# Optimization experiments

Hardware: AMD Instinct MI355X
Metric: run time of the kernel (lower is better)

The kernel has to match this reference:

```python
import jax, jax.numpy as jnp
import numpy as np

B, S, PLM, G = 8, 2048, 768, 256
N_WM, E_WM = 50000, 800000
N_F, E_F = B * S, 131072
K = 4


def _gnn(h, src, dst, Ws, bs, n_nodes):
    # simple GCN-style message passing: aggregate neighbor features via
    # gather (h[src]) + scatter-add (segment_sum), then linear + relu.
    for W, b in zip(Ws, bs):
        m = jax.ops.segment_sum(h[src], dst, num_segments=n_nodes)  # [n, g]
        h = jax.nn.relu((h + m) @ W + b)
    return h


def setup_inputs() -> dict:
    key = jax.random.key(0)
    ks = jax.random.split(key, 16)
    std = 0.02
    inp = {
        "text_embeddings": jax.random.normal(ks[0], (B, S, PLM), jnp.float32),
        "wm_x": jax.random.normal(ks[1], (N_WM, G), jnp.float32),
        "wm_edge_index": jax.random.randint(ks[2], (2, E_WM), 0, N_WM),
        "token2nodepos": jax.random.randint(ks[3], (B * S, K), 0, N_WM),
        "fstm_node_ids": jax.random.randint(ks[4], (N_F,), 0, N_F),
        "fstm_edge_index": jax.random.randint(ks[5], (2, E_F), 0, N_F),
        # extra_emb: nn.Embedding(2, G, padding_idx=0) -> row 0 is zeros
        "extra_emb": jax.random.normal(ks[6], (2, G), jnp.float32).at[0].set(0.0) * std,
        "wm_W1": jax.random.normal(ks[7], (G, G), jnp.float32) * std,
        "wm_b1": jnp.zeros((G,), jnp.float32),
        "wm_W2": jax.random.normal(ks[8], (G, G), jnp.float32) * std,
        "wm_b2": jnp.zeros((G,), jnp.float32),
        "fstm_W1": jax.random.normal(ks[9], (G, G), jnp.float32) * std,
        "fstm_b1": jnp.zeros((G,), jnp.float32),
        "fstm_W2": jax.random.normal(ks[10], (G, G), jnp.float32) * std,
        "fstm_b2": jnp.zeros((G,), jnp.float32),
        "fc1_W": jax.random.normal(ks[11], (G + PLM, G), jnp.float32) * std,
        "fc1_b": jnp.zeros((G,), jnp.float32),
        "fc3_W": jax.random.normal(ks[12], (PLM + 2 * G, PLM), jnp.float32) * std,
        "fc3_b": jnp.zeros((PLM,), jnp.float32),
    }
    return inp


def reference(text_embeddings, wm_x, wm_edge_index, token2nodepos, fstm_node_ids,
              fstm_edge_index, extra_emb, wm_W1, wm_b1, wm_W2, wm_b2,
              fstm_W1, fstm_b1, fstm_W2, fstm_b2, fc1_W, fc1_b, fc3_W, fc3_b):
    # ====== WM ======
    graph_embeddings = _gnn(wm_x, wm_edge_index[0], wm_edge_index[1],
                            (wm_W1, wm_W2), (wm_b1, wm_b2), N_WM)  # [N_WM, G]
    table = jnp.concatenate([extra_emb, graph_embeddings], axis=0)  # [N_WM+2, G]
    # per-token gather-sum over K concept slots (original python loop, vectorized)
    tmp = jnp.sum(table[token2nodepos + 2], axis=1)  # [B*S, G]
    text_flat = text_embeddings.reshape(B * S, PLM)
    graph_text_embed = jnp.concatenate([tmp, text_flat], axis=-1) @ fc1_W + fc1_b  # [B*S, G]
    # ====== FSTM ======
    x = graph_text_embed[fstm_node_ids]  # [B*S, G]
    temporal = _gnn(x, fstm_edge_index[0], fstm_edge_index[1],
                    (fstm_W1, fstm_W2), (fstm_b1, fstm_b2), N_F)
    temporal = temporal.reshape(B, S, G)
    # ====== Final ======
    final_vec = jnp.concatenate(
        [text_embeddings, tmp.reshape(B, S, G), temporal], axis=-1)
    logits = final_vec @ fc3_W + fc3_b  # [B, S, PLM]
    return logits
```

## Files before the change

### kernel.cpp

```cpp
#include <hip/hip_runtime.h>

#define Bsz 8
#define Ssz 2048
#define PLM 768
#define Gd  256
#define N_WM 50000
#define E_WM 800000
#define N_F  16384
#define E_F  131072
#define Kc   4

typedef unsigned short ushort_t;
typedef short short8 __attribute__((ext_vector_type(8)));
typedef float f32x4 __attribute__((ext_vector_type(4)));

__device__ __forceinline__ ushort_t f2bf(float f) {
    union { float f; unsigned int u; } v; v.f = f;
    unsigned int r = (v.u + 0x7fffu + ((v.u >> 16) & 1u)) >> 16;
    return (ushort_t)r;
}
__device__ __forceinline__ float bf2f(ushort_t b) {
    union { unsigned int u; float f; } v; v.u = ((unsigned int)b) << 16;
    return v.f;
}
__device__ __forceinline__ float4 bf4f(ushort4 u) {
    return make_float4(bf2f(u.x), bf2f(u.y), bf2f(u.z), bf2f(u.w));
}

__device__ __forceinline__ void gl2lds16(const ushort_t* g, ushort_t* l) {
    __builtin_amdgcn_global_load_lds(
        (const __attribute__((address_space(1))) unsigned int*)g,
        (__attribute__((address_space(3))) unsigned int*)l, 16, 0, 0);
}

__device__ __forceinline__ void cvt4(const float* __restrict__ in,
                                     ushort_t* __restrict__ out, int i, int n4) {
    if (i < n4) {
        float4 v = ((const float4*)in)[i];
        ushort4 u;
        u.x = f2bf(v.x); u.y = f2bf(v.y); u.z = f2bf(v.z); u.w = f2bf(v.w);
        ((ushort4*)out)[i] = u;
    }
}
__device__ __forceinline__ void wtx(const float* __restrict__ W,
                                    ushort_t* __restrict__ Wt, int K, int N, int idx) {
    if (idx < N * K) {
        int n = idx / K, k = idx % K;
        Wt[idx] = f2bf(W[(size_t)k * N + n]);
    }
}

__global__ void conv_all(const float* __restrict__ wm_x, const float* __restrict__ text,
                         const float* __restrict__ extra,
                         const float* __restrict__ W1, const float* __restrict__ W2,
                         const float* __restrict__ W3, const float* __restrict__ W4,
                         const float* __restrict__ W5, const float* __restrict__ W6,
                         ushort_t* __restrict__ Xb, ushort_t* __restrict__ Tx,
                         ushort_t* __restrict__ Exb,
                         ushort_t* __restrict__ T1, ushort_t* __restrict__ T2,
                         ushort_t* __restrict__ T3, ushort_t* __restrict__ T4,
                         ushort_t* __restrict__ T5, ushort_t* __restrict__ T6) {
    int b = blockIdx.x, t = threadIdx.x;
    if (b < 12500) { cvt4(wm_x, Xb, b * 256 + t, 3200000); return; }
    b -= 12500;
    if (b < 12288) { cvt4(text, Tx, b * 256 + t, 3145728); return; }
    b -= 12288;
    if (b < 1) { cvt4(extra, Exb, t, 128); return; }
    b -= 1;
    if (b < 256) { wtx(W1, T1, 256, 256, b * 256 + t); return; }
    b -= 256;
    if (b < 256) { wtx(W2, T2, 256, 256, b * 256 + t); return; }
    b -= 256;
    if (b < 256) { wtx(W3, T3, 256, 256, b * 256 + t); return; }
    b -= 256;
    if (b < 256) { wtx(W4, T4, 256, 256, b * 256 + t); return; }
    b -= 256;
    if (b < 1024) { wtx(W5, T5, 1024, 256, b * 256 + t); return; }
    b -= 1024;
    wtx(W6, T6, 1280, 768, b * 256 + t);
}

__global__ void hist_both(const int* __restrict__ wm_dst, int* __restrict__ wm_cnt,
                          const int* __restrict__ f_dst, int* __restrict__ fs_cnt) {
    int e = blockIdx.x * 256 + threadIdx.x;
    if (e < E_WM) {
        atomicAdd(&wm_cnt[wm_dst[e]], 1);
    } else {
        int e2 = e - E_WM;
        if (e2 < E_F) atomicAdd(&fs_cnt[f_dst[e2]], 1);
    }
}

__global__ void fill_both(const int* __restrict__ wm_src, const int* __restrict__ wm_dst,
                          int* __restrict__ wm_cur, int* __restrict__ wm_bkt,
                          const int* __restrict__ f_src, const int* __restrict__ f_dst,
                          int* __restrict__ fs_cur, int* __restrict__ fs_bkt) {
    int e = blockIdx.x * 256 + threadIdx.x;
    if (e < E_WM) {
        int p = atomicAdd(&wm_cur[wm_dst[e]], 1);
        wm_bkt[p] = wm_src[e];
    } else {
        int e2 = e - E_WM;
        if (e2 < E_F) {
            int p = atomicAdd(&fs_cur[f_dst[e2]], 1);
            fs_bkt[p] = f_src[e2];
        }
    }
}

__device__ __forceinline__ void scan1_body(const int* __restrict__ cnt,
                                           int* __restrict__ bsum, int n, int lb,
                                           int* sm) {
    int t = threadIdx.x;
    int base = lb * 1024 + t * 4;
    int s = 0;
    if (base + 3 < n) {
        int4 q = *(const int4*)&cnt[base];
        s = q.x + q.y + q.z + q.w;
    } else {
#pragma unroll
        for (int i = 0; i < 4; ++i) if (base + i < n) s += cnt[base + i];
    }
    sm[t] = s; __syncthreads();
#pragma unroll
    for (int st = 128; st > 0; st >>= 1) {
        if (t < st) sm[t] += sm[t + st];
        __syncthreads();
    }
    if (t == 0) bsum[lb] = sm[0];
}

#define NBW 49
#define NBF 16
__global__ __launch_bounds__(256) void scan1_both(const int* __restrict__ wm_cnt,
                                                  int* __restrict__ bsum_wm,
                                                  const int* __restrict__ fs_cnt,
                                                  int* __restrict__ bsum_fs) {
    __shared__ int sm[256];
    int b = blockIdx.x;
    if (b < NBW) scan1_body(wm_cnt, bsum_wm, N_WM, b, sm);
    else         scan1_body(fs_cnt, bsum_fs, N_F, b - NBW, sm);
}

__global__ void scan_bsums_both(int* __restrict__ bw, int* __restrict__ bf) {
    int w = threadIdx.x >> 6, lane = threadIdx.x & 63;
    int* b = w ? bf : bw;
    int nb = w ? NBF : NBW;
    int o = (lane < nb) ? b[lane] : 0;
    int v = o;
#pragma unroll
    for (int off = 1; off < 64; off <<= 1) {
        int t = __shfl_up(v, off, 64);
        if (lane >= off) v += t;
    }
    if (lane < nb) b[lane] = v - o;
}

__device__ __forceinline__ void scan2_body(int* __restrict__ cnt, int* __restrict__ off,
                                           const int* __restrict__ bsum, int n,
                                           int total, int lb, int* sm) {
    int t = threadIdx.x;
    int base = lb * 1024 + t * 4;
    int v0 = 0, v1 = 0, v2 = 0, v3 = 0;
    if (base + 3 < n) {
        int4 q = *(const int4*)&cnt[base];
        v0 = q.x; v1 = q.y; v2 = q.z; v3 = q.w;
    } else {
        if (base + 0 < n) v0 = cnt[base + 0];
        if (base + 1 < n) v1 = cnt[base + 1];
        if (base + 2 < n) v2 = cnt[base + 2];
        if (base + 3 < n) v3 = cnt[base + 3];
    }
    int s = v0 + v1 + v2 + v3;
    sm[t] = s;
    __syncthreads();
#pragma unroll
    for (int st = 1; st < 256; st <<= 1) {
        int x = (t >= st) ? sm[t - st] : 0;
        __syncthreads();
        sm[t] += x;
        __syncthreads();
    }
    int ex = bsum[lb] + sm[t] - s;
    int o0 = ex, o1 = ex + v0, o2 = o1 + v1, o3 = o2 + v2;
    if (base + 0 < n) { off[base + 0] = o0; cnt[base + 0] = o0; }
    if (base + 1 < n) { off[base + 1] = o1; cnt[base + 1] = o1; }
    if (base + 2 < n) { off[base + 2] = o2; cnt[base + 2] = o2; }
    if (base + 3 < n) { off[base + 3] = o3; cnt[base + 3] = o3; }
    if (lb == 0 && t == 0) off[n] = total;
}

__global__ __launch_bounds__(256) void scan2_both(int* __restrict__ wm_cnt,
                                                  int* __restrict__ wm_off,
                                                  const int* __restrict__ bsum_wm,
                                                  int* __restrict__ fs_cnt,
                                                  int* __restrict__ fs_off,
                                                  const int* __restrict__ bsum_fs) {
    __shared__ int sm[256];
    int b = blockIdx.x;
    if (b < NBW) scan2_body(wm_cnt, wm_off, bsum_wm, N_WM, E_WM, b, sm);
    else         scan2_body(fs_cnt, fs_off, bsum_fs, N_F, E_F, b - NBW, sm);
}

__global__ void aggregate_kernel(const ushort_t* __restrict__ h,
                                 const int* __restrict__ off,
                                 const int* __restrict__ bucket,
                                 ushort_t* __restrict__ hm, int n) {
    int i = blockIdx.x * 4 + (threadIdx.x >> 6);
    if (i >= n) return;
    int lane = threadIdx.x & 63;
    int s0 = off[i], s1 = off[i + 1];
    const ushort4* hp = (const ushort4*)h;
    float4 acc = bf4f(hp[(size_t)i * 64 + lane]);
    int j = s0;
    for (; j + 8 <= s1; j += 8) {
        int b0 = bucket[j + 0], b1 = bucket[j + 1];
        int b2 = bucket[j + 2], b3 = bucket[j + 3];
        int b4 = bucket[j + 4], b5 = bucket[j + 5];
        int b6 = bucket[j + 6], b7 = bucket[j + 7];
        ushort4 r0 = hp[(size_t)b0 * 64 + lane];
        ushort4 r1 = hp[(size_t)b1 * 64 + lane];
        ushort4 r2 = hp[(size_t)b2 * 64 + lane];
        ushort4 r3 = hp[(size_t)b3 * 64 + lane];
        ushort4 r4 = hp[(size_t)b4 * 64 + lane];
        ushort4 r5 = hp[(size_t)b5 * 64 + lane];
        ushort4 r6 = hp[(size_t)b6 * 64 + lane];
        ushort4 r7 = hp[(size_t)b7 * 64 + lane];
        float4 v0 = bf4f(r0), v1 = bf4f(r1), v2 = bf4f(r2), v3 = bf4f(r3);
        float4 v4 = bf4f(r4), v5 = bf4f(r5), v6 = bf4f(r6), v7 = bf4f(r7);
        acc.x += v0.x + v1.x + v2.x + v3.x + v4.x + v5.x + v6.x + v7.x;
        acc.y += v0.y + v1.y + v2.y + v3.y + v4.y + v5.y + v6.y + v7.y;
        acc.z += v0.z + v1.z + v2.z + v3.z + v4.z + v5.z + v6.z + v7.z;
        acc.w += v0.w + v1.w + v2.w + v3.w + v4.w + v5.w + v6.w + v7.w;
    }
    for (; j + 2 <= s1; j += 2) {
        int b0 = bucket[j + 0], b1 = bucket[j + 1];
        ushort4 r0 = hp[(size_t)b0 * 64 + lane];
        ushort4 r1 = hp[(size_t)b1 * 64 + lane];
        float4 v0 = bf4f(r0), v1 = bf4f(r1);
        acc.x += v0.x + v1.x; acc.y += v0.y + v1.y;
        acc.z += v0.z + v1.z; acc.w += v0.w + v1.w;
    }
    if (j < s1) {
        int b0 = bucket[j];
        float4 v0 = bf4f(hp[(size_t)b0 * 64 + lane]);
        acc.x += v0.x; acc.y += v0.y; acc.z += v0.z; acc.w += v0.w;
    }
    ushort4 u;
    u.x = f2bf(acc.x); u.y = f2bf(acc.y); u.z = f2bf(acc.z); u.w = f2bf(acc.w);
    ((ushort4*)hm)[(size_t)i * 64 + lane] = u;
}

__global__ void tmp_kernel(const ushort_t* __restrict__ gemb,
                           const ushort_t* __restrict__ extra,
                           const int* __restrict__ t2np,
                           ushort_t* __restrict__ D) {
    int i = blockIdx.x * 4 + (threadIdx.x >> 6);
    int lane = threadIdx.x & 63;
    float4 s = make_float4(0.f, 0.f, 0.f, 0.f);
#pragma unroll
    for (int k = 0; k < Kc; ++k) {
        int idx = t2np[i * Kc + k] + 2;
        const ushort4* row = (idx < 2) ? (const ushort4*)(extra + (size_t)idx * Gd)
                                       : (const ushort4*)(gemb + (size_t)(idx - 2) * Gd);
        float4 v = bf4f(row[lane]);
        s.x += v.x; s.y += v.y; s.z += v.z; s.w += v.w;
    }
    ushort4 u;
    u.x = f2bf(s.x); u.y = f2bf(s.y); u.z = f2bf(s.z); u.w = f2bf(s.w);
    ((ushort4*)D)[(size_t)i * 64 + lane] = u;
}

__global__ void gather_kernel(const ushort_t* __restrict__ Ein,
                              const int* __restrict__ ids,
                              ushort_t* __restrict__ F) {
    int i = blockIdx.x * 4 + (threadIdx.x >> 6);
    int lane = threadIdx.x & 63;
    ((ushort4*)F)[(size_t)i * 64 + lane] =
        ((const ushort4*)Ein)[(size_t)ids[i] * 64 + lane];
}

#define TBM 128
#define TBN 128
#define TBK 64

__device__ __forceinline__ void xcd_swizzle(int& bx, int& by) {
    int gx = gridDim.x;
    int nwg = gx * gridDim.y;
    int orig = by * gx + bx;
    int q = nwg >> 3, r = nwg & 7;
    int xcd = orig & 7, loc = orig >> 3;
    int wg = (xcd < r ? xcd * (q + 1) : r * (q + 1) + (xcd - r) * q) + loc;
    bx = wg % gx;
    by = wg / gx;
}

template <int MODE, int OUTBF>
__global__ __launch_bounds__(256) void mfma_gemm(
    const ushort_t* __restrict__ p0, const ushort_t* __restrict__ p1,
    const ushort_t* __restrict__ p2, const ushort_t* __restrict__ Wt,
    const float* __restrict__ bias, void* __restrict__ Cv,
    int M, int N, int K, int relu) {
    __shared__ ushort_t As[TBM * TBK];
    __shared__ ushort_t Bs[TBN * TBK];

    int tid  = threadIdx.x;
    int lane = tid & 63;
    int wave = tid >> 6;
    int wm = (wave >> 1) * 64, wn = (wave & 1) * 64;
    int bx = blockIdx.x, by = blockIdx.y;
    xcd_swizzle(bx, by);
    int row0 = by * TBM, col0 = bx * TBN;
    int l15 = lane & 15, l4 = lane >> 4;

    f32x4 acc[4][4];
#pragma unroll
    for (int i = 0; i < 4; ++i)
#pragma unroll
        for (int j = 0; j < 4; ++j)
            acc[i][j] = (f32x4){0.f, 0.f, 0.f, 0.f};

    for (int k0 = 0; k0 < K; k0 += TBK) {
#pragma unroll
        for (int it = 0; it < 4; ++it) {
            int eb = it * 2048 + wave * 512;
            int le = eb + lane * 8;
            int r  = le >> 6;
            int kl = le & 63;
            int grow = row0 + r; if (grow > M - 1) grow = M - 1;
            int gk = k0 + kl;
            const ushort_t* gp;
            if (MODE == 0)
                gp = p0 + (size_t)grow * K + gk;
            else if (MODE == 2)
                gp = (gk < 256) ? p0 + (size_t)grow * 256 + gk
                                : p1 + (size_t)grow * 768 + (gk - 256);
            else
                gp = (gk < 768) ? p0 + (size_t)grow * 768 + gk
                   : (gk < 1024) ? p1 + (size_t)grow * 256 + (gk - 768)
                                 : p2 + (size_t)grow * 256 + (gk - 1024);
            gl2lds16(gp, &As[eb]);
        }
#pragma unroll
        for (int it = 0; it < 4; ++it) {
            int eb = it * 2048 + wave * 512;
            int le = eb + lane * 8;
            int nl = le >> 6;
            int kl = le & 63;
            const ushort_t* gp = Wt + (size_t)(col0 + nl) * K + k0 + kl;
            gl2lds16(gp, &Bs[eb]);
        }
        __syncthreads();

#pragma unroll
        for (int ks = 0; ks < TBK; ks += 32) {
            short8 af[4], bfr[4];
#pragma unroll
            for (int mi = 0; mi < 4; ++mi)
                af[mi] = *(const short8*)&As[(wm + mi * 16 + l15) * TBK + ks + l4 * 8];
#pragma unroll
            for (int ni = 0; ni < 4; ++ni)
                bfr[ni] = *(const short8*)&Bs[(wn + ni * 16 + l15) * TBK + ks + l4 * 8];
#pragma unroll
            for (int mi = 0; mi < 4; ++mi)
#pragma unroll
                for (int ni = 0; ni < 4; ++ni)
                    acc[mi][ni] = __builtin_amdgcn_mfma_f32_16x16x32_bf16(
                        af[mi], bfr[ni], acc[mi][ni], 0, 0, 0);
        }
        __syncthreads();
    }

#pragma unroll
    for (int ni = 0; ni < 4; ++ni) {
        int c = col0 + wn + ni * 16 + l15;
        float bv = bias[c];
#pragma unroll
        for (int mi = 0; mi < 4; ++mi) {
#pragma unroll
            for (int r = 0; r < 4; ++r) {
                int rr = row0 + wm + mi * 16 + l4 * 4 + r;
                if (rr < M) {
                    float v = acc[mi][ni][r] + bv;
                    if (relu) v = fmaxf(v, 0.f);
                    if (OUTBF) ((ushort_t*)Cv)[(size_t)rr * N + c] = f2bf(v);
                    else       ((float*)Cv)[(size_t)rr * N + c] = v;
                }
            }
        }
    }
}

extern "C" void kernel_launch(void* const* d_in, const int* in_sizes, int n_in,
                              void* d_out, int out_size, void* d_ws, size_t ws_size,
                              hipStream_t stream) {
    const float* text    = (const float*)d_in[0];
    const float* wm_x    = (const float*)d_in[1];
    const int*   wm_ei   = (const int*)d_in[2];
    const int*   t2np    = (const int*)d_in[3];
    const int*   f_ids   = (const int*)d_in[4];
    const int*   f_ei    = (const int*)d_in[5];
    const float* extra   = (const float*)d_in[6];
    const float* wm_W1   = (const float*)d_in[7];
    const float* wm_b1   = (const float*)d_in[8];
    const float* wm_W2   = (const float*)d_in[9];
    const float* wm_b2   = (const float*)d_in[10];
    const float* fs_W1   = (const float*)d_in[11];
    const float* fs_b1   = (const float*)d_in[12];
    const float* fs_W2   = (const float*)d_in[13];
    const float* fs_b2   = (const float*)d_in[14];
    const float* fc1_W   = (const float*)d_in[15];
    const float* fc1_b   = (const float*)d_in[16];
    const float* fc3_W   = (const float*)d_in[17];
    const float* fc3_b   = (const float*)d_in[18];
    float* out = (float*)d_out;

    ushort_t* Xb  = (ushort_t*)d_ws;
    ushort_t* Ag  = Xb + 12800000;
    ushort_t* Gm  = Ag + 12800000;
    ushort_t* Tx  = Gm + 12800000;
    ushort_t* Dt  = Tx + 12582912;
    ushort_t* Ee  = Dt + 4194304;
    ushort_t* Wv  = Ee + 4194304;
    ushort_t* wt_wm1 = Wv;
    ushort_t* wt_wm2 = wt_wm1 + 65536;
    ushort_t* wt_fs1 = wt_wm2 + 65536;
    ushort_t* wt_fs2 = wt_fs1 + 65536;
    ushort_t* wt_fc1 = wt_fs2 + 65536;
    ushort_t* wt_fc3 = wt_fc1 + 262144;
    ushort_t* Exb    = wt_fc3 + 983040;
    int* wm_off = (int*)(Exb + 512);
    int* fs_off = wm_off + N_WM + 1;
    int* wm_cnt = fs_off + N_F + 1;
    int* fs_cnt = wm_cnt + N_WM;
    int* wm_bkt = fs_cnt + N_F;
    int* fs_bkt = wm_bkt + E_WM;
    int* bsum_wm = fs_bkt + E_F;
    int* bsum_fs = bsum_wm + 64;

    ushort_t* h1 = Xb;
    ushort_t* F  = Gm;
    ushort_t* H  = Gm + 4194304;
    ushort_t* T  = Ee;

    const int* wm_src = wm_ei;
    const int* wm_dst = wm_ei + E_WM;
    const int* f_src  = f_ei;
    const int* f_dst  = f_ei + E_F;

    dim3 blk(256);
    dim3 gW(Gd / TBN, (N_WM + TBM - 1) / TBM);
    dim3 gF(Gd / TBN, N_F / TBM);
    dim3 gO(PLM / TBN, N_F / TBM);

    const int nbE = (E_WM + E_F) / 256;

    hipMemsetAsync(wm_cnt, 0, (N_WM + N_F) * sizeof(int), stream);
    hist_both<<<nbE, blk, 0, stream>>>(wm_dst, wm_cnt, f_dst, fs_cnt);
    scan1_both<<<NBW + NBF, blk, 0, stream>>>(wm_cnt, bsum_wm, fs_cnt, bsum_fs);
    scan_bsums_both<<<1, 128, 0, stream>>>(bsum_wm, bsum_fs);
    scan2_both<<<NBW + NBF, blk, 0, stream>>>(wm_cnt, wm_off, bsum_wm,
                                              fs_cnt, fs_off, bsum_fs);
    fill_both<<<nbE, blk, 0, stream>>>(wm_src, wm_dst, wm_cnt, wm_bkt,
                                       f_src, f_dst, fs_cnt, fs_bkt);

    conv_all<<<30677, blk, 0, stream>>>(wm_x, text, extra,
                                        wm_W1, wm_W2, fs_W1, fs_W2, fc1_W, fc3_W,
                                        Xb, Tx, Exb,
                                        wt_wm1, wt_wm2, wt_fs1, wt_fs2,
                                        wt_fc1, wt_fc3);

    aggregate_kernel<<<(N_WM + 3) / 4, blk, 0, stream>>>(Xb, wm_off, wm_bkt, Ag, N_WM);
    mfma_gemm<0, 1><<<gW, blk, 0, stream>>>(Ag, nullptr, nullptr, wt_wm1, wm_b1,
                                            h1, N_WM, Gd, Gd, 1);
    aggregate_kernel<<<(N_WM + 3) / 4, blk, 0, stream>>>(h1, wm_off, wm_bkt, Ag, N_WM);
    mfma_gemm<0, 1><<<gW, blk, 0, stream>>>(Ag, nullptr, nullptr, wt_wm2, wm_b2,
                                            Gm, N_WM, Gd, Gd, 1);
    tmp_kernel<<<N_F / 4, blk, 0, stream>>>(Gm, Exb, t2np, Dt);
    mfma_gemm<2, 1><<<gF, blk, 0, stream>>>(Dt, Tx, nullptr, wt_fc1, fc1_b,
                                            Ee, N_F, Gd, Gd + PLM, 0);
    gather_kernel<<<N_F / 4, blk, 0, stream>>>(Ee, f_ids, F);
    aggregate_kernel<<<N_F / 4, blk, 0, stream>>>(F, fs_off, fs_bkt, Ag, N_F);
    mfma_gemm<0, 1><<<gF, blk, 0, stream>>>(Ag, nullptr, nullptr, wt_fs1, fs_b1,
                                            H, N_F, Gd, Gd, 1);
    aggregate_kernel<<<N_F / 4, blk, 0, stream>>>(H, fs_off, fs_bkt, Ag, N_F);
    mfma_gemm<0, 1><<<gF, blk, 0, stream>>>(Ag, nullptr, nullptr, wt_fs2, fs_b2,
                                            T, N_F, Gd, Gd, 1);
    mfma_gemm<3, 0><<<gO, blk, 0, stream>>>(Tx, Dt, T, wt_fc3, fc3_b,
                                            out, N_F, PLM, PLM + 2 * Gd, 0);
}
```

Before: 634.3 us.

## Build CSR via two-level bucketed counting sort with shared-memory atomics

Replaces the global-atomic histogram, three-pass scan and global-atomic fill with a two-level radix-style counting sort. Edges are first bucketed by high bits of the destination into coarse buckets using shared-memory histograms per chunk, then each coarse bucket is sorted locally in shared memory to produce offsets and bucket arrays. The aim is to cut contended global atomics and random scattered writes during CSR construction. The cost is an extra pass through an int2 staging buffer that reuses the Ag workspace, plus more kernel launches.

```diff
diff --git a/kernel.cpp b/kernel.cpp
--- a/kernel.cpp
+++ b/kernel.cpp
@@ -80,100 +80,48 @@
     wtx(W6, T6, 1280, 768, b * 256 + t);
 }
 
-__global__ void hist_both(const int* __restrict__ wm_dst, int* __restrict__ wm_cnt,
-                          const int* __restrict__ f_dst, int* __restrict__ fs_cnt) {
-    int e = blockIdx.x * 256 + threadIdx.x;
-    if (e < E_WM) {
-        atomicAdd(&wm_cnt[wm_dst[e]], 1);
+#define WM_P 512
+#define WM_CH 1563
+#define WM_SHIFT 8
+#define FS_P 128
+#define FS_CH 1024
+#define FS_SHIFT 6
+
+__global__ __launch_bounds__(256) void csr_p1(const int* __restrict__ wm_dst,
+                                              const int* __restrict__ f_dst,
+                                              int* __restrict__ Cwm,
+                                              int* __restrict__ Cfs) {
+    __shared__ int hist[256];
+    int b = blockIdx.x, t = threadIdx.x;
+    hist[t] = 0; __syncthreads();
+    if (b < WM_P) {
+        int e0 = b * WM_CH, e1 = e0 + WM_CH; if (e1 > E_WM) e1 = E_WM;
+        for (int e = e0 + t; e < e1; e += 256)
+            atomicAdd(&hist[wm_dst[e] >> WM_SHIFT], 1);
+        __syncthreads();
+        Cwm[b * 256 + t] = hist[t];
     } else {
-        int e2 = e - E_WM;
-        if (e2 < E_F) atomicAdd(&fs_cnt[f_dst[e2]], 1);
-    }
-}
-
-__global__ void fill_both(const int* __restrict__ wm_src, const int* __restrict__ wm_dst,
-                          int* __restrict__ wm_cur, int* __restrict__ wm_bkt,
-                          const int* __restrict__ f_src, const int* __restrict__ f_dst,
-                          int* __restrict__ fs_cur, int* __restrict__ fs_bkt) {
-    int e = blockIdx.x * 256 + threadIdx.x;
-    if (e < E_WM) {
-        int p = atomicAdd(&wm_cur[wm_dst[e]], 1);
-        wm_bkt[p] = wm_src[e];
-    } else {
-        int e2 = e - E_WM;
-        if (e2 < E_F) {
-            int p = atomicAdd(&fs_cur[f_dst[e2]], 1);
-            fs_bkt[p] = f_src[e2];
-        }
-    }
-}
-
-__device__ __forceinline__ void scan1_body(const int* __restrict__ cnt,
-                                           int* __restrict__ bsum, int n, int lb,
-                                           int* sm) {
-    int t = threadIdx.x;
-    int base = lb * 1024 + t * 4;
-    int s = 0;
-    if (base + 3 < n) {
-        int4 q = *(const int4*)&cnt[base];
-        s = q.x + q.y + q.z + q.w;
-    } else {
-#pragma unroll
-        for (int i = 0; i < 4; ++i) if (base + i < n) s += cnt[base + i];
-    }
+        int p = b - WM_P;
+        int e0 = p * FS_CH, e1 = e0 + FS_CH;
+        for (int e = e0 + t; e < e1; e += 256)
+            atomicAdd(&hist[f_dst[e] >> FS_SHIFT], 1);
+        __syncthreads();
+        Cfs[p * 256 + t] = hist[t];
+    }
+}
+
+__global__ __launch_bounds__(256) void csr_p2a(int* __restrict__ Cwm, int* __restrict__ BTwm,
+                                               int* __restrict__ Cfs, int* __restrict__ BTfs) {
+    __shared__ int sm[256];
+    int b = blockIdx.x, t = threadIdx.x;
+    int* C; int* BT; int P; int bk;
+    if (b < 256) { C = Cwm; BT = BTwm; P = WM_P; bk = b; }
+    else         { C = Cfs; BT = BTfs; P = FS_P; bk = b - 256; }
+    int half = P >> 1;
+    int v0 = 0, v1 = 0;
+    if (t < half) { v0 = C[(2 * t) * 256 + bk]; v1 = C[(2 * t + 1) * 256 + bk]; }
+    int s = v0 + v1;
     sm[t] = s; __syncthreads();
-#pragma unroll
-    for (int st = 128; st > 0; st >>= 1) {
-        if (t < st) sm[t] += sm[t + st];
-        __syncthreads();
-    }
-    if (t == 0) bsum[lb] = sm[0];
-}
-
-#define NBW 49
-#define NBF 16
-__global__ __launch_bounds__(256) void scan1_both(const int* __restrict__ wm_cnt,
-                                                  int* __restrict__ bsum_wm,
-                                                  const int* __restrict__ fs_cnt,
-                                                  int* __restrict__ bsum_fs) {
-    __shared__ int sm[256];
-    int b = blockIdx.x;
-    if (b < NBW) scan1_body(wm_cnt, bsum_wm, N_WM, b, sm);
-    else         scan1_body(fs_cnt, bsum_fs, N_F, b - NBW, sm);
-}
-
-__global__ void scan_bsums_both(int* __restrict__ bw, int* __restrict__ bf) {
-    int w = threadIdx.x >> 6, lane = threadIdx.x & 63;
-    int* b = w ? bf : bw;
-    int nb = w ? NBF : NBW;
-    int o = (lane < nb) ? b[lane] : 0;
-    int v = o;
-#pragma unroll
-    for (int off = 1; off < 64; off <<= 1) {
-        int t = __shfl_up(v, off, 64);
-        if (lane >= off) v += t;
-    }
-    if (lane < nb) b[lane] = v - o;
-}
-
-__device__ __forceinline__ void scan2_body(int* __restrict__ cnt, int* __restrict__ off,
-                                           const int* __restrict__ bsum, int n,
-                                           int total, int lb, int* sm) {
-    int t = threadIdx.x;
-    int base = lb * 1024 + t * 4;
-    int v0 = 0, v1 = 0, v2 = 0, v3 = 0;
-    if (base + 3 < n) {
-        int4 q = *(const int4*)&cnt[base];
-        v0 = q.x; v1 = q.y; v2 = q.z; v3 = q.w;
-    } else {
-        if (base + 0 < n) v0 = cnt[base + 0];
-        if (base + 1 < n) v1 = cnt[base + 1];
-        if (base + 2 < n) v2 = cnt[base + 2];
-        if (base + 3 < n) v3 = cnt[base + 3];
-    }
-    int s = v0 + v1 + v2 + v3;
-    sm[t] = s;
-    __syncthreads();
 #pragma unroll
     for (int st = 1; st < 256; st <<= 1) {
         int x = (t >= st) ? sm[t - st] : 0;
@@ -181,25 +129,112 @@
         sm[t] += x;
         __syncthreads();
     }
-    int ex = bsum[lb] + sm[t] - s;
-    int o0 = ex, o1 = ex + v0, o2 = o1 + v1, o3 = o2 + v2;
-    if (base + 0 < n) { off[base + 0] = o0; cnt[base + 0] = o0; }
-    if (base + 1 < n) { off[base + 1] = o1; cnt[base + 1] = o1; }
-    if (base + 2 < n) { off[base + 2] = o2; cnt[base + 2] = o2; }
-    if (base + 3 < n) { off[base + 3] = o3; cnt[base + 3] = o3; }
-    if (lb == 0 && t == 0) off[n] = total;
-}
-
-__global__ __launch_bounds__(256) void scan2_both(int* __restrict__ wm_cnt,
-                                                  int* __restrict__ wm_off,
-                                                  const int* __restrict__ bsum_wm,
-                                                  int* __restrict__ fs_cnt,
-                                                  int* __restrict__ fs_off,
-                                                  const int* __restrict__ bsum_fs) {
+    int ex = sm[t] - s;
+    if (t < half) {
+        C[(2 * t) * 256 + bk] = ex;
+        C[(2 * t + 1) * 256 + bk] = ex + v0;
+    }
+    if (t == 255) BT[bk] = sm[255];
+}
+
+__global__ __launch_bounds__(256) void csr_p2b(const int* __restrict__ BTwm,
+                                               int* __restrict__ BSwm,
+                                               const int* __restrict__ BTfs,
+                                               int* __restrict__ BSfs) {
     __shared__ int sm[256];
-    int b = blockIdx.x;
-    if (b < NBW) scan2_body(wm_cnt, wm_off, bsum_wm, N_WM, E_WM, b, sm);
-    else         scan2_body(fs_cnt, fs_off, bsum_fs, N_F, E_F, b - NBW, sm);
+    int t = threadIdx.x;
+    const int* BT = blockIdx.x ? BTfs : BTwm;
+    int* BS = blockIdx.x ? BSfs : BSwm;
+    int E = blockIdx.x ? E_F : E_WM;
+    int v = BT[t];
+    sm[t] = v; __syncthreads();
+#pragma unroll
+    for (int st = 1; st < 256; st <<= 1) {
+        int x = (t >= st) ? sm[t - st] : 0;
+        __syncthreads();
+        sm[t] += x;
+        __syncthreads();
+    }
+    BS[t] = sm[t] - v;
+    if (t == 255) BS[256] = E;
+}
+
+__global__ __launch_bounds__(256) void csr_p3(const int* __restrict__ wm_src,
+                                              const int* __restrict__ wm_dst,
+                                              const int* __restrict__ Cwm,
+                                              const int* __restrict__ BSwm,
+                                              int2* __restrict__ SEwm,
+                                              const int* __restrict__ f_src,
+                                              const int* __restrict__ f_dst,
+                                              const int* __restrict__ Cfs,
+                                              const int* __restrict__ BSfs,
+                                              int2* __restrict__ SEfs) {
+    __shared__ int cur[256];
+    int b = blockIdx.x, t = threadIdx.x;
+    if (b < WM_P) {
+        cur[t] = Cwm[b * 256 + t] + BSwm[t];
+        __syncthreads();
+        int e0 = b * WM_CH, e1 = e0 + WM_CH; if (e1 > E_WM) e1 = E_WM;
+        for (int e = e0 + t; e < e1; e += 256) {
+            int d = wm_dst[e], s = wm_src[e];
+            int pos = atomicAdd(&cur[d >> WM_SHIFT], 1);
+            SEwm[pos] = make_int2(s, d);
+        }
+    } else {
+        int p = b - WM_P;
+        cur[t] = Cfs[p * 256 + t] + BSfs[t];
+        __syncthreads();
+        int e0 = p * FS_CH, e1 = e0 + FS_CH;
+        for (int e = e0 + t; e < e1; e += 256) {
+            int d = f_dst[e], s = f_src[e];
+            int pos = atomicAdd(&cur[d >> FS_SHIFT], 1);
+            SEfs[pos] = make_int2(s, d);
+        }
+    }
+}
+
+__global__ __launch_bounds__(256) void csr_p4(const int2* __restrict__ SEwm,
+                                              const int* __restrict__ BSwm,
+                                              int* __restrict__ wm_off,
+                                              int* __restrict__ wm_bkt,
+                                              const int2* __restrict__ SEfs,
+                                              const int* __restrict__ BSfs,
+                                              int* __restrict__ fs_off,
+                                              int* __restrict__ fs_bkt) {
+    __shared__ int cnt[256];
+    __shared__ int sm[256];
+    int ob = blockIdx.x, t = threadIdx.x;
+    const int2* SE; const int* BS; int* off; int* bkt;
+    int b, nb0, n, E, bw;
+    if (ob < 256) { SE = SEwm; BS = BSwm; off = wm_off; bkt = wm_bkt;
+                    b = ob; nb0 = b << WM_SHIFT; n = N_WM; E = E_WM; bw = 256; }
+    else          { SE = SEfs; BS = BSfs; off = fs_off; bkt = fs_bkt;
+                    b = ob - 256; nb0 = b << FS_SHIFT; n = N_F; E = E_F; bw = 64; }
+    int e0 = BS[b], e1 = BS[b + 1];
+    cnt[t] = 0; __syncthreads();
+    for (int e = e0 + t; e < e1; e += 256)
+        atomicAdd(&cnt[SE[e].y - nb0], 1);
+    __syncthreads();
+    int v = cnt[t];
+    sm[t] = v; __syncthreads();
+#pragma unroll
+    for (int st = 1; st < 256; st <<= 1) {
+        int x = (t >= st) ? sm[t - st] : 0;
+        __syncthreads();
+        sm[t] += x;
+        __syncthreads();
+    }
+    int ex = sm[t] - v;
+    if (t < bw && nb0 + t < n) off[nb0 + t] = e0 + ex;
+    if (b == 0 && t == 0) off[n] = E;
+    __syncthreads();
+    cnt[t] = e0 + ex;
+    __syncthreads();
+    for (int e = e0 + t; e < e1; e += 256) {
+        int2 sd = SE[e];
+        int pos = atomicAdd(&cnt[sd.y - nb0], 1);
+        bkt[pos] = sd.x;
+    }
 }
 
 __global__ void aggregate_kernel(const ushort_t* __restrict__ h,
@@ -431,12 +466,16 @@
     ushort_t* Exb    = wt_fc3 + 983040;
     int* wm_off = (int*)(Exb + 512);
     int* fs_off = wm_off + N_WM + 1;
-    int* wm_cnt = fs_off + N_F + 1;
-    int* fs_cnt = wm_cnt + N_WM;
-    int* wm_bkt = fs_cnt + N_F;
+    int* wm_bkt = fs_off + N_F + 1;
     int* fs_bkt = wm_bkt + E_WM;
-    int* bsum_wm = fs_bkt + E_F;
-    int* bsum_fs = bsum_wm + 64;
+    int2* SEwm = (int2*)Ag;
+    int2* SEfs = SEwm + E_WM;
+    int*  Cwm  = (int*)(SEfs + E_F);
+    int*  Cfs  = Cwm + WM_P * 256;
+    int*  BTwm = Cfs + FS_P * 256;
+    int*  BTfs = BTwm + 256;
+    int*  BSwm = BTfs + 256;
+    int*  BSfs = BSwm + 257;
 
     ushort_t* h1 = Xb;
     ushort_t* F  = Gm;
@@ -453,16 +492,13 @@
     dim3 gF(Gd / TBN, N_F / TBM);
     dim3 gO(PLM / TBN, N_F / TBM);
 
-    const int nbE = (E_WM + E_F) / 256;
-
-    hipMemsetAsync(wm_cnt, 0, (N_WM + N_F) * sizeof(int), stream);
-    hist_both<<<nbE, blk, 0, stream>>>(wm_dst, wm_cnt, f_dst, fs_cnt);
-    scan1_both<<<NBW + NBF, blk, 0, stream>>>(wm_cnt, bsum_wm, fs_cnt, bsum_fs);
-    scan_bsums_both<<<1, 128, 0, stream>>>(bsum_wm, bsum_fs);
-    scan2_both<<<NBW + NBF, blk, 0, stream>>>(wm_cnt, wm_off, bsum_wm,
-                                              fs_cnt, fs_off, bsum_fs);
-    fill_both<<<nbE, blk, 0, stream>>>(wm_src, wm_dst, wm_cnt, wm_bkt,
-                                       f_src, f_dst, fs_cnt, fs_bkt);
+    csr_p1<<<WM_P + FS_P, blk, 0, stream>>>(wm_dst, f_dst, Cwm, Cfs);
+    csr_p2a<<<512, blk, 0, stream>>>(Cwm, BTwm, Cfs, BTfs);
+    csr_p2b<<<2, blk, 0, stream>>>(BTwm, BSwm, BTfs, BSfs);
+    csr_p3<<<WM_P + FS_P, blk, 0, stream>>>(wm_src, wm_dst, Cwm, BSwm, SEwm,
+                                            f_src, f_dst, Cfs, BSfs, SEfs);
+    csr_p4<<<512, blk, 0, stream>>>(SEwm, BSwm, wm_off, wm_bkt,
+                                    SEfs, BSfs, fs_off, fs_bkt);
 
     conv_all<<<30677, blk, 0, stream>>>(wm_x, text, extra,
                                         wm_W1, wm_W2, fs_W1, fs_W2, fc1_W, fc3_W,
```

After: 556.0 us. 1.14x faster.
